# Kernel optimization log

Measured on AMD Instinct MI355X. Metric: run time of the kernel, lower is better.

The kernel has to match this reference:

```python
import jax, jax.numpy as jnp
import numpy as np

H = 16
D_MODEL = 1024
D_K = D_MODEL // H
B, S = 4, 2048


def setup_inputs() -> dict:
    key = jax.random.key(0)
    ks = jax.random.split(key, 8)
    scale = 1.0 / np.sqrt(D_MODEL)
    return {
        "query": jax.random.normal(ks[0], (B, S, D_MODEL), dtype=jnp.float32),
        "key": jax.random.normal(ks[1], (B, S, D_MODEL), dtype=jnp.float32),
        "value": jax.random.normal(ks[2], (B, S, D_MODEL), dtype=jnp.float32),
        "A": jnp.zeros((1,), dtype=jnp.float32),
        "Wq": jax.random.normal(ks[3], (D_MODEL, D_MODEL), dtype=jnp.float32) * scale,
        "bq": jnp.zeros((D_MODEL,), dtype=jnp.float32),
        "Wk": jax.random.normal(ks[4], (D_MODEL, D_MODEL), dtype=jnp.float32) * scale,
        "bk": jnp.zeros((D_MODEL,), dtype=jnp.float32),
        "Wv": jax.random.normal(ks[5], (D_MODEL, D_MODEL), dtype=jnp.float32) * scale,
        "bv": jnp.zeros((D_MODEL,), dtype=jnp.float32),
        "Wo": jax.random.normal(ks[6], (D_MODEL, D_MODEL), dtype=jnp.float32) * scale,
        "bo": jnp.zeros((D_MODEL,), dtype=jnp.float32),
    }


def reference(query, key, value, A, Wq, bq, Wk, bk, Wv, bv, Wo, bo):
    nb = query.shape[0]

    def proj(x, W, b):
        # torch Linear: x @ W.T + b, then view(B, S, H, D_K) and transpose -> [B, H, S, D_K]
        y = jnp.einsum('bsd,ed->bse', x, W) + b
        return y.reshape(nb, -1, H, D_K).transpose(0, 2, 1, 3)

    q = proj(query, Wq, bq)
    k = proj(key, Wk, bk)
    v = proj(value, Wv, bv)

    # NOTE: original code has NO 1/sqrt(d_k) scaling, no mask, no dropout.
    scores = jnp.einsum('bhqd,bhkd->bhqk', q, k)  # [B,H,S,S]
    p_attn = jax.nn.softmax(scores, axis=-1)
    x = jnp.einsum('bhqk,bhkd->bhqd', p_attn, v)  # [B,H,S,D_K]

    x = x.transpose(0, 2, 1, 3).reshape(nb, -1, H * D_K)  # [B,S,d_model]
    out = jnp.einsum('bsd,ed->bse', x, Wo) + bo
    loss = jnp.asarray(0.0, dtype=out.dtype)
    return (out, loss)
```

## Files before the change

### kernel.cpp

```cpp
#include <hip/hip_runtime.h>

typedef unsigned short u16;
typedef _Float16 half8 __attribute__((ext_vector_type(8)));
typedef _Float16 h2 __attribute__((ext_vector_type(2)));
typedef float f32x4 __attribute__((ext_vector_type(4)));
typedef u16 u16x4 __attribute__((ext_vector_type(4)));
typedef u16 u16x8 __attribute__((ext_vector_type(8)));

#define MFMAH(a, b, c) __builtin_amdgcn_mfma_f32_16x16x32_f16(a, b, c, 0, 0, 0)

constexpr float LOG2E = 1.44269504088896f;
constexpr float THR = 12.0f;

__device__ __forceinline__ u16 f2h(float f) {
  _Float16 h = (_Float16)f;
  return __builtin_bit_cast(u16, h);
}
__device__ __forceinline__ h2 pkrtz(float a, float b) {
  return __builtin_bit_cast(h2, __builtin_amdgcn_cvt_pkrtz(a, b));
}

__device__ __forceinline__ void gload_lds16(const void* g, void* l) {
  __builtin_amdgcn_global_load_lds(
      (const __attribute__((address_space(1))) void*)g,
      (__attribute__((address_space(3))) void*)l,
      16, 0, 0);
}

__device__ __forceinline__ void conv_block(const float* __restrict__ in,
                                           u16* __restrict__ out, int i) {
  const float4 a = reinterpret_cast<const float4*>(in)[2 * i];
  const float4 b = reinterpret_cast<const float4*>(in)[2 * i + 1];
  u16x8 o;
  o[0] = f2h(a.x); o[1] = f2h(a.y); o[2] = f2h(a.z); o[3] = f2h(a.w);
  o[4] = f2h(b.x); o[5] = f2h(b.y); o[6] = f2h(b.z); o[7] = f2h(b.w);
  reinterpret_cast<u16x8*>(out)[i] = o;
}

__global__ __launch_bounds__(256) void conv_w4(const float* __restrict__ w0,
                                               const float* __restrict__ w1,
                                               const float* __restrict__ w2,
                                               const float* __restrict__ w3,
                                               u16* __restrict__ o0, u16* __restrict__ o1,
                                               u16* __restrict__ o2, u16* __restrict__ o3,
                                               int n8) {
  int i = blockIdx.x * 256 + threadIdx.x;
  const int stride = gridDim.x * 256;
  for (; i < 4 * n8; i += stride) {
    const int sel = i / n8, j = i - sel * n8;
    if (sel == 0) conv_block(w0, o0, j);
    else if (sel == 1) conv_block(w1, o1, j);
    else if (sel == 2) conv_block(w2, o2, j);
    else conv_block(w3, o3, j);
  }
}

template <int MODE, bool A32>
__global__ __launch_bounds__(256) void gemm_bt(const void* __restrict__ Av,
                                               const u16* __restrict__ Bw,
                                               const float* __restrict__ bias,
                                               void* __restrict__ Cv,
                                               int M, int N, int K, float scale) {
  __shared__ u16 As[128 * 32];
  __shared__ u16 Bs[128 * 32];
  const int tid = threadIdx.x;
  const int lane = tid & 63;
  const int l16 = lane & 15, lhi = lane >> 4;
  const int wid = tid >> 6;
  const int wm = wid >> 1, wn = wid & 1;
  const int id = blockIdx.x + blockIdx.y * gridDim.x;
  const int xcd = id & 7, slot = id >> 3;
  const int by = ((slot & 7) << 3) | xcd;
  const int bx = slot >> 3;
  const int bm0 = by * 128;
  const int bn0 = bx * 128;

  const int c0 = tid, c1 = tid + 256;
  const u16* A16 = (const u16*)Av;
  const float* Af = (const float*)Av;
  const u16* Ag0 = A16 + (size_t)(bm0 + (c0 >> 2)) * K + (c0 & 3) * 8;
  const u16* Ag1 = A16 + (size_t)(bm0 + (c1 >> 2)) * K + (c1 & 3) * 8;
  const u16* Bg0 = Bw + (size_t)(bn0 + (c0 >> 2)) * K + (c0 & 3) * 8;
  const u16* Bg1 = Bw + (size_t)(bn0 + (c1 >> 2)) * K + (c1 & 3) * 8;
  const float* Ar = Af + (size_t)(bm0 + (tid >> 1)) * K + (tid & 1) * 16;
  u16* AsW = &As[(tid >> 1) * 32 + (tid & 1) * 16];

  f32x4 acc[4][4] = {};

  for (int kt = 0; kt < K; kt += 32) {
    if constexpr (A32) {
      const float4 a0 = *reinterpret_cast<const float4*>(Ar + kt);
      const float4 a1 = *reinterpret_cast<const float4*>(Ar + kt + 4);
      const float4 a2 = *reinterpret_cast<const float4*>(Ar + kt + 8);
      const float4 a3 = *reinterpret_cast<const float4*>(Ar + kt + 12);
      gload_lds16(Bg0 + kt, &Bs[c0 * 8]);
      gload_lds16(Bg1 + kt, &Bs[c1 * 8]);
      union { u16x8 u; h2 h[4]; } w0, w1;
      w0.h[0] = pkrtz(a0.x, a0.y); w0.h[1] = pkrtz(a0.z, a0.w);
      w0.h[2] = pkrtz(a1.x, a1.y); w0.h[3] = pkrtz(a1.z, a1.w);
      w1.h[0] = pkrtz(a2.x, a2.y); w1.h[1] = pkrtz(a2.z, a2.w);
      w1.h[2] = pkrtz(a3.x, a3.y); w1.h[3] = pkrtz(a3.z, a3.w);
      *reinterpret_cast<u16x8*>(AsW) = w0.u;
      *reinterpret_cast<u16x8*>(AsW + 8) = w1.u;
    } else {
      gload_lds16(Ag0 + kt, &As[c0 * 8]);
      gload_lds16(Ag1 + kt, &As[c1 * 8]);
      gload_lds16(Bg0 + kt, &Bs[c0 * 8]);
      gload_lds16(Bg1 + kt, &Bs[c1 * 8]);
    }
    __syncthreads();
    half8 af[4], bf[4];
#pragma unroll
    for (int f = 0; f < 4; ++f)
      af[f] = *reinterpret_cast<const half8*>(&As[(wm * 64 + f * 16 + l16) * 32 + lhi * 8]);
#pragma unroll
    for (int f = 0; f < 4; ++f)
      bf[f] = *reinterpret_cast<const half8*>(&Bs[(wn * 64 + f * 16 + l16) * 32 + lhi * 8]);
#pragma unroll
    for (int i = 0; i < 4; ++i)
#pragma unroll
      for (int j = 0; j < 4; ++j)
        acc[i][j] = MFMAH(af[i], bf[j], acc[i][j]);
    __syncthreads();
  }

#pragma unroll
  for (int i = 0; i < 4; ++i) {
    const int m0 = bm0 + wm * 64 + i * 16 + lhi * 4;
#pragma unroll
    for (int j = 0; j < 4; ++j) {
      const int n = bn0 + wn * 64 + j * 16 + l16;
      const float bb = bias[n];
      if (MODE == 0) {
        float* Cf = (float*)Cv;
#pragma unroll
        for (int r = 0; r < 4; ++r)
          Cf[(size_t)(m0 + r) * N + n] = acc[i][j][r] + bb;
      } else if (MODE == 2) {
        u16* C = (u16*)Cv;
        u16x4 pack;
#pragma unroll
        for (int r = 0; r < 4; ++r) pack[r] = f2h(acc[i][j][r] + bb);
        const int head = (m0 >> 11) * 16 + (n >> 6);
        const int s0 = m0 & 2047;
        const int d = n & 63;
        const int within =
            ((s0 >> 5) & 1) * 2048 + d * 32 + ((s0 >> 2) & 3) * 8 + ((s0 >> 4) & 1) * 4;
        const int sw = within ^ ((d & 7) << 3);
        const size_t idx = (size_t)head * 131072 + (size_t)(s0 >> 6) * 4096 + sw;
        *reinterpret_cast<u16x4*>(&C[idx]) = pack;
      } else {
        u16* C = (u16*)Cv;
#pragma unroll
        for (int r = 0; r < 4; ++r) {
          const int m = m0 + r;
          const size_t idx =
              ((size_t)((m >> 11) * 16 + (n >> 6)) * 2048 + (m & 2047)) * 64 + (n & 63);
          C[idx] = f2h((acc[i][j][r] + bb) * scale);
        }
      }
    }
  }
  if (MODE == 0) {
    if (id == 0 && tid == 0)
      ((float*)Cv)[(size_t)M * N] = 0.0f;
  }
}

__global__ __launch_bounds__(256, 4) void attn_fwd(const u16* __restrict__ Q,
                                                   const u16* __restrict__ Kh,
                                                   const u16* __restrict__ VL,
                                                   u16* __restrict__ X) {
  __shared__ u16 Ks[2][4096];
  __shared__ u16 Vs[2][4096];

  const int tid = threadIdx.x, lane = tid & 63, w = tid >> 6;
  const int l16 = lane & 15, lhi = lane >> 4;
  const int blk = blockIdx.x;
  const int xcd = blk & 7, wi = blk >> 3;
  const int bh = (xcd << 3) | (wi >> 4);
  const int qt = wi & 15;
  const int b = bh >> 4, h = bh & 15;

  const size_t qrow0 = (size_t)bh * 2048 + qt * 128 + w * 32;
  half8 qf[2][2];
#pragma unroll
  for (int fq = 0; fq < 2; ++fq)
#pragma unroll
    for (int ks = 0; ks < 2; ++ks)
      qf[fq][ks] = *reinterpret_cast<const half8*>(
          &Q[(qrow0 + fq * 16 + l16) * 64 + ks * 32 + lhi * 8]);

  f32x4 o[2][4] = {};
  float mrow[2] = {-1e30f, -1e30f};
  float ssum[2] = {0.0f, 0.0f};

  const u16* Kb = Kh + (size_t)bh * 2048 * 64;
  const u16* VLh = VL + (size_t)bh * 64 * 64 * 32;

#define STAGE_KV(bufidx, tt)                                                      \
  do {                                                                            \
    const int kb0_ = (tt) * 64;                                                   \
    _Pragma("unroll")                                                             \
    for (int ii_ = 0; ii_ < 2; ++ii_) {                                           \
      const int c_ = tid + ii_ * 256;                                             \
      const int r_ = c_ >> 3, cb_ = c_ & 7;                                       \
      gload_lds16(Kb + (size_t)(kb0_ + r_) * 64 + ((cb_ ^ (r_ & 7)) << 3),        \
                  &Ks[bufidx][c_ * 8]);                                           \
      gload_lds16(VLh + (size_t)(tt) * 4096 + c_ * 8, &Vs[bufidx][c_ * 8]);       \
    }                                                                             \
  } while (0)

  STAGE_KV(0, 0);
  __syncthreads();

  for (int t = 0; t < 32; ++t) {
    const int cur = t & 1;
    if (t < 31) STAGE_KV(cur ^ 1, t + 1);
    f32x4 sc[2][4] = {};
    __builtin_amdgcn_s_setprio(1);
#pragma unroll
    for (int fk = 0; fk < 4; ++fk) {
      const int row = fk * 16 + l16;
#pragma unroll
      for (int ks = 0; ks < 2; ++ks) {
        const int off = (row * 64 + ks * 32 + lhi * 8) ^ ((row & 7) << 3);
        const half8 kf = *reinterpret_cast<const half8*>(&Ks[cur][off]);
#pragma unroll
        for (int fq = 0; fq < 2; ++fq) sc[fq][fk] = MFMAH(kf, qf[fq][ks], sc[fq][fk]);
      }
    }
    __builtin_amdgcn_s_setprio(0);
    float lm[2];
#pragma unroll
    for (int fq = 0; fq < 2; ++fq) {
      float a0 = fmaxf(fmaxf(sc[fq][0][0], sc[fq][0][1]), sc[fq][0][2]);
      float a1 = fmaxf(fmaxf(sc[fq][0][3], sc[fq][1][0]), sc[fq][1][1]);
      float a2 = fmaxf(fmaxf(sc[fq][1][2], sc[fq][1][3]), sc[fq][2][0]);
      float a3 = fmaxf(fmaxf(sc[fq][2][1], sc[fq][2][2]), sc[fq][2][3]);
      float a4 = fmaxf(fmaxf(sc[fq][3][0], sc[fq][3][1]), sc[fq][3][2]);
      float b0 = fmaxf(fmaxf(a0, a1), a2);
      float b1 = fmaxf(fmaxf(a3, a4), sc[fq][3][3]);
      lm[fq] = fmaxf(b0, b1);
    }
    const int trig = (lm[0] > mrow[0] + THR) || (lm[1] > mrow[1] + THR);
    if (__any(trig)) {
#pragma unroll
      for (int fq = 0; fq < 2; ++fq) {
        float rm = lm[fq];
        rm = fmaxf(rm, __shfl_xor(rm, 16));
        rm = fmaxf(rm, __shfl_xor(rm, 32));
        const float nm = fmaxf(mrow[fq], rm);
        const float scl = __builtin_amdgcn_exp2f(mrow[fq] - nm);
        mrow[fq] = nm;
        ssum[fq] *= scl;
        float sb[4];
#pragma unroll
        for (int r = 0; r < 4; ++r) sb[r] = __shfl(scl, lhi * 4 + r);
#pragma unroll
        for (int fd = 0; fd < 4; ++fd)
#pragma unroll
          for (int r = 0; r < 4; ++r) o[fq][fd][r] *= sb[r];
      }
    }
    half8 pa2[2][2];
#pragma unroll
    for (int fq = 0; fq < 2; ++fq) {
      union { half8 v[2]; h2 hh[8]; } uu;
#pragma unroll
      for (int fk = 0; fk < 4; ++fk) {
        const float p0 = __builtin_amdgcn_exp2f(sc[fq][fk][0] - mrow[fq]);
        const float p1 = __builtin_amdgcn_exp2f(sc[fq][fk][1] - mrow[fq]);
        const float p2 = __builtin_amdgcn_exp2f(sc[fq][fk][2] - mrow[fq]);
        const float p3 = __builtin_amdgcn_exp2f(sc[fq][fk][3] - mrow[fq]);
        ssum[fq] += (p0 + p1) + (p2 + p3);
        uu.hh[fk * 2 + 0] = pkrtz(p0, p1);
        uu.hh[fk * 2 + 1] = pkrtz(p2, p3);
      }
      pa2[fq][0] = uu.v[0];
      pa2[fq][1] = uu.v[1];
    }
    __builtin_amdgcn_s_setprio(1);
#pragma unroll
    for (int fd = 0; fd < 4; ++fd)
#pragma unroll
      for (int ts = 0; ts < 2; ++ts) {
        const int va = (ts * 2048 + (fd * 16 + l16) * 32 + lhi * 8) ^ ((l16 & 7) << 3);
        const half8 vf = *reinterpret_cast<const half8*>(&Vs[cur][va]);
#pragma unroll
        for (int fq = 0; fq < 2; ++fq) o[fq][fd] = MFMAH(pa2[fq][ts], vf, o[fq][fd]);
      }
    __builtin_amdgcn_s_setprio(0);
    __syncthreads();
  }
#undef STAGE_KV

#pragma unroll
  for (int fq = 0; fq < 2; ++fq) {
    float ss = ssum[fq];
    ss += __shfl_xor(ss, 16);
    ss += __shfl_xor(ss, 32);
    float iv[4];
#pragma unroll
    for (int r = 0; r < 4; ++r) iv[r] = 1.0f / __shfl(ss, lhi * 4 + r);
#pragma unroll
    for (int r = 0; r < 4; ++r) {
      const int q = qt * 128 + w * 32 + fq * 16 + lhi * 4 + r;
#pragma unroll
      for (int fd = 0; fd < 4; ++fd) {
        const int col = h * 64 + fd * 16 + l16;
        X[((size_t)b * 2048 + q) * 1024 + col] = f2h(o[fq][fd][r] * iv[r]);
      }
    }
  }
}

extern "C" void kernel_launch(void* const* d_in, const int* in_sizes, int n_in,
                              void* d_out, int out_size, void* d_ws, size_t ws_size,
                              hipStream_t stream) {
  const float* q_f  = (const float*)d_in[0];
  const float* k_f  = (const float*)d_in[1];
  const float* v_f  = (const float*)d_in[2];
  const float* Wq_f = (const float*)d_in[4];
  const float* bq   = (const float*)d_in[5];
  const float* Wk_f = (const float*)d_in[6];
  const float* bk   = (const float*)d_in[7];
  const float* Wv_f = (const float*)d_in[8];
  const float* bv   = (const float*)d_in[9];
  const float* Wo_f = (const float*)d_in[10];
  const float* bo   = (const float*)d_in[11];

  const int SZ = 4 * 2048 * 1024;
  const int SW = 1024 * 1024;

  u16* ws = (u16*)d_ws;
  u16* wqb = ws;
  u16* wkb = wqb + SW;
  u16* wvb = wkb + SW;
  u16* wob = wvb + SW;
  u16* Qb  = wob + SW;
  u16* Kb  = Qb + SZ;
  u16* VLb = Kb + SZ;
  u16* Xb  = VLb + SZ;
  const size_t need_bytes = (size_t)(4 * SZ + 4 * SW) * 2;
  if (ws_size < need_bytes) return;

  conv_w4<<<1024, 256, 0, stream>>>(Wq_f, Wk_f, Wv_f, Wo_f, wqb, wkb, wvb, wob, SW / 8);

  dim3 gg(1024 / 128, 8192 / 128);
  gemm_bt<1, true><<<gg, 256, 0, stream>>>(q_f, wqb, bq, Qb, 8192, 1024, 1024, LOG2E);
  gemm_bt<1, true><<<gg, 256, 0, stream>>>(k_f, wkb, bk, Kb, 8192, 1024, 1024, 1.0f);
  gemm_bt<2, true><<<gg, 256, 0, stream>>>(v_f, wvb, bv, VLb, 8192, 1024, 1024, 1.0f);

  attn_fwd<<<dim3(1024), 256, 0, stream>>>(Qb, Kb, VLb, Xb);

  gemm_bt<0, false><<<gg, 256, 0, stream>>>(Xb, wob, bo, d_out, 8192, 1024, 1024, 1.0f);
}
```

Baseline: 244.5 us.

## Double-buffer projection GEMMs and merge Q/K/V projections into one launch

Replaces the templated GEMM with two specialized kernels. Both use double-buffered LDS so the next K-tile's global loads (fp32 A into registers, f16 B via direct-to-LDS loads) overlap the current tile's MFMAs, and each iteration needs one barrier instead of two. The three Q/K/V projections are folded into a single 3D-grid launch, which removes two launch gaps and gives the GPU one larger wave of blocks. The cost is double the LDS footprint, which may lower occupancy, plus more live registers for the prefetched A values.

```diff
diff --git a/kernel.cpp b/kernel.cpp
--- a/kernel.cpp
+++ b/kernel.cpp
@@ -19,7 +19,6 @@
 __device__ __forceinline__ h2 pkrtz(float a, float b) {
   return __builtin_bit_cast(h2, __builtin_amdgcn_cvt_pkrtz(a, b));
 }
-
 __device__ __forceinline__ void gload_lds16(const void* g, void* l) {
   __builtin_amdgcn_global_load_lds(
       (const __attribute__((address_space(1))) void*)g,
@@ -55,74 +54,94 @@
   }
 }
 
-template <int MODE, bool A32>
-__global__ __launch_bounds__(256) void gemm_bt(const void* __restrict__ Av,
-                                               const u16* __restrict__ Bw,
-                                               const float* __restrict__ bias,
-                                               void* __restrict__ Cv,
-                                               int M, int N, int K, float scale) {
-  __shared__ u16 As[128 * 32];
-  __shared__ u16 Bs[128 * 32];
+__global__ __launch_bounds__(256) void proj_gemm(
+    const float* __restrict__ Aq, const float* __restrict__ Ak, const float* __restrict__ Avv,
+    const u16* __restrict__ Wq, const u16* __restrict__ Wk, const u16* __restrict__ Wv,
+    const float* __restrict__ bq, const float* __restrict__ bk, const float* __restrict__ bv,
+    u16* __restrict__ Cq, u16* __restrict__ Ck, u16* __restrict__ Cvv) {
+  __shared__ u16 As[2][4096];
+  __shared__ u16 Bs[2][4096];
   const int tid = threadIdx.x;
-  const int lane = tid & 63;
-  const int l16 = lane & 15, lhi = lane >> 4;
-  const int wid = tid >> 6;
-  const int wm = wid >> 1, wn = wid & 1;
-  const int id = blockIdx.x + blockIdx.y * gridDim.x;
-  const int xcd = id & 7, slot = id >> 3;
+  const int lane = tid & 63, l16 = lane & 15, lhi = lane >> 4;
+  const int wid = tid >> 6, wm = wid >> 1, wn = wid & 1;
+  const int id = blockIdx.x + (blockIdx.y << 3) + (blockIdx.z << 9);
+  const int xcd = id & 7;
+  const int slot = id >> 3;
   const int by = ((slot & 7) << 3) | xcd;
-  const int bx = slot >> 3;
-  const int bm0 = by * 128;
-  const int bn0 = bx * 128;
+  const int rest = slot >> 3;
+  const int bx = rest & 7;
+  const int z = rest >> 3;
+  const int bm0 = by * 128, bn0 = bx * 128;
+
+  const float* Af = (z == 0) ? Aq : ((z == 1) ? Ak : Avv);
+  const u16* Bw = (z == 0) ? Wq : ((z == 1) ? Wk : Wv);
+  const float* bias = (z == 0) ? bq : ((z == 1) ? bk : bv);
+  u16* C = (z == 0) ? Cq : ((z == 1) ? Ck : Cvv);
+  const float scale = (z == 0) ? LOG2E : 1.0f;
 
   const int c0 = tid, c1 = tid + 256;
-  const u16* A16 = (const u16*)Av;
-  const float* Af = (const float*)Av;
-  const u16* Ag0 = A16 + (size_t)(bm0 + (c0 >> 2)) * K + (c0 & 3) * 8;
-  const u16* Ag1 = A16 + (size_t)(bm0 + (c1 >> 2)) * K + (c1 & 3) * 8;
-  const u16* Bg0 = Bw + (size_t)(bn0 + (c0 >> 2)) * K + (c0 & 3) * 8;
-  const u16* Bg1 = Bw + (size_t)(bn0 + (c1 >> 2)) * K + (c1 & 3) * 8;
-  const float* Ar = Af + (size_t)(bm0 + (tid >> 1)) * K + (tid & 1) * 16;
-  u16* AsW = &As[(tid >> 1) * 32 + (tid & 1) * 16];
+  const u16* Bg0 = Bw + (size_t)(bn0 + (c0 >> 2)) * 1024 + (c0 & 3) * 8;
+  const u16* Bg1 = Bw + (size_t)(bn0 + (c1 >> 2)) * 1024 + (c1 & 3) * 8;
+  const float* Ar = Af + (size_t)(bm0 + (tid >> 1)) * 1024 + (tid & 1) * 16;
+  u16* AsW0 = &As[0][(tid >> 1) * 32 + (tid & 1) * 16];
+  u16* AsW1 = &As[1][(tid >> 1) * 32 + (tid & 1) * 16];
 
   f32x4 acc[4][4] = {};
-
-  for (int kt = 0; kt < K; kt += 32) {
-    if constexpr (A32) {
-      const float4 a0 = *reinterpret_cast<const float4*>(Ar + kt);
-      const float4 a1 = *reinterpret_cast<const float4*>(Ar + kt + 4);
-      const float4 a2 = *reinterpret_cast<const float4*>(Ar + kt + 8);
-      const float4 a3 = *reinterpret_cast<const float4*>(Ar + kt + 12);
-      gload_lds16(Bg0 + kt, &Bs[c0 * 8]);
-      gload_lds16(Bg1 + kt, &Bs[c1 * 8]);
-      union { u16x8 u; h2 h[4]; } w0, w1;
-      w0.h[0] = pkrtz(a0.x, a0.y); w0.h[1] = pkrtz(a0.z, a0.w);
-      w0.h[2] = pkrtz(a1.x, a1.y); w0.h[3] = pkrtz(a1.z, a1.w);
-      w1.h[0] = pkrtz(a2.x, a2.y); w1.h[1] = pkrtz(a2.z, a2.w);
-      w1.h[2] = pkrtz(a3.x, a3.y); w1.h[3] = pkrtz(a3.z, a3.w);
-      *reinterpret_cast<u16x8*>(AsW) = w0.u;
-      *reinterpret_cast<u16x8*>(AsW + 8) = w1.u;
-    } else {
-      gload_lds16(Ag0 + kt, &As[c0 * 8]);
-      gload_lds16(Ag1 + kt, &As[c1 * 8]);
-      gload_lds16(Bg0 + kt, &Bs[c0 * 8]);
-      gload_lds16(Bg1 + kt, &Bs[c1 * 8]);
-    }
-    __syncthreads();
+  float4 an[4];
+
+#define LOADA(kt)                                            \
+  do {                                                       \
+    an[0] = *reinterpret_cast<const float4*>(Ar + (kt));     \
+    an[1] = *reinterpret_cast<const float4*>(Ar + (kt) + 4); \
+    an[2] = *reinterpret_cast<const float4*>(Ar + (kt) + 8); \
+    an[3] = *reinterpret_cast<const float4*>(Ar + (kt) + 12);\
+  } while (0)
+#define STAGEB(buf, kt)                                      \
+  do {                                                       \
+    gload_lds16(Bg0 + (kt), &Bs[buf][c0 * 8]);               \
+    gload_lds16(Bg1 + (kt), &Bs[buf][c1 * 8]);               \
+  } while (0)
+#define WRITEA(buf)                                          \
+  do {                                                       \
+    union { u16x8 u; h2 h[4]; } w0_, w1_;                    \
+    w0_.h[0] = pkrtz(an[0].x, an[0].y); w0_.h[1] = pkrtz(an[0].z, an[0].w); \
+    w0_.h[2] = pkrtz(an[1].x, an[1].y); w0_.h[3] = pkrtz(an[1].z, an[1].w); \
+    w1_.h[0] = pkrtz(an[2].x, an[2].y); w1_.h[1] = pkrtz(an[2].z, an[2].w); \
+    w1_.h[2] = pkrtz(an[3].x, an[3].y); w1_.h[3] = pkrtz(an[3].z, an[3].w); \
+    u16* dst_ = (buf) ? AsW1 : AsW0;                         \
+    *reinterpret_cast<u16x8*>(dst_) = w0_.u;                 \
+    *reinterpret_cast<u16x8*>(dst_ + 8) = w1_.u;             \
+  } while (0)
+
+  LOADA(0);
+  STAGEB(0, 0);
+  WRITEA(0);
+  __syncthreads();
+
+  for (int ki = 0; ki < 32; ++ki) {
+    const int cur = ki & 1, nxt = cur ^ 1;
+    if (ki < 31) {
+      LOADA((ki + 1) * 32);
+      STAGEB(nxt, (ki + 1) * 32);
+    }
     half8 af[4], bf[4];
 #pragma unroll
     for (int f = 0; f < 4; ++f)
-      af[f] = *reinterpret_cast<const half8*>(&As[(wm * 64 + f * 16 + l16) * 32 + lhi * 8]);
+      af[f] = *reinterpret_cast<const half8*>(&As[cur][(wm * 64 + f * 16 + l16) * 32 + lhi * 8]);
 #pragma unroll
     for (int f = 0; f < 4; ++f)
-      bf[f] = *reinterpret_cast<const half8*>(&Bs[(wn * 64 + f * 16 + l16) * 32 + lhi * 8]);
+      bf[f] = *reinterpret_cast<const half8*>(&Bs[cur][(wn * 64 + f * 16 + l16) * 32 + lhi * 8]);
 #pragma unroll
     for (int i = 0; i < 4; ++i)
 #pragma unroll
       for (int j = 0; j < 4; ++j)
         acc[i][j] = MFMAH(af[i], bf[j], acc[i][j]);
+    if (ki < 31) WRITEA(nxt);
     __syncthreads();
   }
+#undef LOADA
+#undef STAGEB
+#undef WRITEA
 
 #pragma unroll
   for (int i = 0; i < 4; ++i) {
@@ -131,13 +150,7 @@
     for (int j = 0; j < 4; ++j) {
       const int n = bn0 + wn * 64 + j * 16 + l16;
       const float bb = bias[n];
-      if (MODE == 0) {
-        float* Cf = (float*)Cv;
-#pragma unroll
-        for (int r = 0; r < 4; ++r)
-          Cf[(size_t)(m0 + r) * N + n] = acc[i][j][r] + bb;
-      } else if (MODE == 2) {
-        u16* C = (u16*)Cv;
+      if (z == 2) {
         u16x4 pack;
 #pragma unroll
         for (int r = 0; r < 4; ++r) pack[r] = f2h(acc[i][j][r] + bb);
@@ -150,7 +163,6 @@
         const size_t idx = (size_t)head * 131072 + (size_t)(s0 >> 6) * 4096 + sw;
         *reinterpret_cast<u16x4*>(&C[idx]) = pack;
       } else {
-        u16* C = (u16*)Cv;
 #pragma unroll
         for (int r = 0; r < 4; ++r) {
           const int m = m0 + r;
@@ -161,10 +173,73 @@
       }
     }
   }
-  if (MODE == 0) {
-    if (id == 0 && tid == 0)
-      ((float*)Cv)[(size_t)M * N] = 0.0f;
-  }
+}
+
+__global__ __launch_bounds__(256) void out_gemm(const u16* __restrict__ A,
+                                                const u16* __restrict__ Bw,
+                                                const float* __restrict__ bias,
+                                                float* __restrict__ C) {
+  __shared__ u16 As[2][4096];
+  __shared__ u16 Bs[2][4096];
+  const int tid = threadIdx.x;
+  const int lane = tid & 63, l16 = lane & 15, lhi = lane >> 4;
+  const int wid = tid >> 6, wm = wid >> 1, wn = wid & 1;
+  const int id = blockIdx.x + (blockIdx.y << 3);
+  const int xcd = id & 7, slot = id >> 3;
+  const int by = ((slot & 7) << 3) | xcd;
+  const int bx = slot >> 3;
+  const int bm0 = by * 128, bn0 = bx * 128;
+
+  const int c0 = tid, c1 = tid + 256;
+  const u16* Ag0 = A + (size_t)(bm0 + (c0 >> 2)) * 1024 + (c0 & 3) * 8;
+  const u16* Ag1 = A + (size_t)(bm0 + (c1 >> 2)) * 1024 + (c1 & 3) * 8;
+  const u16* Bg0 = Bw + (size_t)(bn0 + (c0 >> 2)) * 1024 + (c0 & 3) * 8;
+  const u16* Bg1 = Bw + (size_t)(bn0 + (c1 >> 2)) * 1024 + (c1 & 3) * 8;
+
+  f32x4 acc[4][4] = {};
+
+#define STAGE16(buf, kt)                                  \
+  do {                                                    \
+    gload_lds16(Ag0 + (kt), &As[buf][c0 * 8]);            \
+    gload_lds16(Ag1 + (kt), &As[buf][c1 * 8]);            \
+    gload_lds16(Bg0 + (kt), &Bs[buf][c0 * 8]);            \
+    gload_lds16(Bg1 + (kt), &Bs[buf][c1 * 8]);            \
+  } while (0)
+
+  STAGE16(0, 0);
+  __syncthreads();
+  for (int ki = 0; ki < 32; ++ki) {
+    const int cur = ki & 1;
+    if (ki < 31) STAGE16(cur ^ 1, (ki + 1) * 32);
+    half8 af[4], bf[4];
+#pragma unroll
+    for (int f = 0; f < 4; ++f)
+      af[f] = *reinterpret_cast<const half8*>(&As[cur][(wm * 64 + f * 16 + l16) * 32 + lhi * 8]);
+#pragma unroll
+    for (int f = 0; f < 4; ++f)
+      bf[f] = *reinterpret_cast<const half8*>(&Bs[cur][(wn * 64 + f * 16 + l16) * 32 + lhi * 8]);
+#pragma unroll
+    for (int i = 0; i < 4; ++i)
+#pragma unroll
+      for (int j = 0; j < 4; ++j)
+        acc[i][j] = MFMAH(af[i], bf[j], acc[i][j]);
+    __syncthreads();
+  }
+#undef STAGE16
+
+#pragma unroll
+  for (int i = 0; i < 4; ++i) {
+    const int m0 = bm0 + wm * 64 + i * 16 + lhi * 4;
+#pragma unroll
+    for (int j = 0; j < 4; ++j) {
+      const int n = bn0 + wn * 64 + j * 16 + l16;
+      const float bb = bias[n];
+#pragma unroll
+      for (int r = 0; r < 4; ++r)
+        C[(size_t)(m0 + r) * 1024 + n] = acc[i][j][r] + bb;
+    }
+  }
+  if (id == 0 && tid == 0) C[(size_t)8192 * 1024] = 0.0f;
 }
 
 __global__ __launch_bounds__(256, 4) void attn_fwd(const u16* __restrict__ Q,
@@ -347,12 +422,10 @@
 
   conv_w4<<<1024, 256, 0, stream>>>(Wq_f, Wk_f, Wv_f, Wo_f, wqb, wkb, wvb, wob, SW / 8);
 
-  dim3 gg(1024 / 128, 8192 / 128);
-  gemm_bt<1, true><<<gg, 256, 0, stream>>>(q_f, wqb, bq, Qb, 8192, 1024, 1024, LOG2E);
-  gemm_bt<1, true><<<gg, 256, 0, stream>>>(k_f, wkb, bk, Kb, 8192, 1024, 1024, 1.0f);
-  gemm_bt<2, true><<<gg, 256, 0, stream>>>(v_f, wvb, bv, VLb, 8192, 1024, 1024, 1.0f);
+  proj_gemm<<<dim3(8, 64, 3), 256, 0, stream>>>(q_f, k_f, v_f, wqb, wkb, wvb,
+                                                bq, bk, bv, Qb, Kb, VLb);
 
   attn_fwd<<<dim3(1024), 256, 0, stream>>>(Qb, Kb, VLb, Xb);
 
-  gemm_bt<0, false><<<gg, 256, 0, stream>>>(Xb, wob, bo, d_out, 8192, 1024, 1024, 1.0f);
-}
+  out_gemm<<<dim3(8, 64), 256, 0, stream>>>(Xb, wob, bo, (float*)d_out);
+}
```

Result: faster. 214.8 us (-12.2%).
